# Kernel tuning notes

Hardware: AMD Instinct MI355X
Metric: run time of the kernel (lower is better)

The kernel has to match this reference:

```python
import jax, jax.numpy as jnp
import numpy as np

B, C, H, W = 32, 1024, 32, 32  # N = H*W must equal C for the attn_c * attn_s broadcast
C8 = C // 8


def setup_inputs() -> dict:
    key = jax.random.key(0)
    ks = jax.random.split(key, 9)
    s = 1.0 / np.sqrt(C)
    return {
        "z": jax.random.normal(ks[0], (B, C, H, W), jnp.float32),
        "x": jax.random.normal(ks[1], (B, C, H, W), jnp.float32),
        "y": jax.random.normal(ks[2], (B, C, H, W), jnp.float32),
        "Wq": jax.random.normal(ks[3], (C8, C), jnp.float32) * s,
        "bq": jax.random.normal(ks[4], (C8,), jnp.float32) * 0.01,
        "Wk": jax.random.normal(ks[5], (C8, C), jnp.float32) * s,
        "bk": jax.random.normal(ks[6], (C8,), jnp.float32) * 0.01,
        "Wv": jax.random.normal(ks[7], (C, C), jnp.float32) * s,
        "bv": jax.random.normal(ks[8], (C,), jnp.float32) * 0.01,
    }


def reference(z, x, y, Wq, bq, Wk, bk, Wv, bv):
    b, c, h, w = x.shape
    n = h * w
    xf = x.reshape(b, c, n)
    yf = y.reshape(b, c, n)
    zf = z.reshape(b, c, n)

    # 1x1 convs == channel matmuls
    q = jnp.einsum('oc,bcn->bon', Wq, xf) + bq[None, :, None]   # (B, C/8, N)
    k = jnp.einsum('oc,bcn->bon', Wk, yf) + bk[None, :, None]   # (B, C/8, N)

    # channel-projected spatial attention: (B, N, N)
    energy_c = jnp.einsum('bcn,bcm->bnm', q, k)
    attention_c = jax.nn.softmax(energy_c, axis=-1)

    # raw channel attention: (B, C, C)
    energy_s = jnp.einsum('bcn,bdn->bcd', xf, yf)
    energy_s = jnp.max(energy_s, axis=-1, keepdims=True) - energy_s
    attention_s = jax.nn.softmax(energy_s, axis=-1)

    # multiplicative combine + third softmax (requires N == C)
    attention = jax.nn.softmax(attention_c * attention_s, axis=-1)

    v = jnp.einsum('oc,bcn->bon', Wv, zf) + bv[None, :, None]   # (B, C, N)
    # out[b,c,m] = sum_n v[b,c,n] * attention[b,m,n]  (value @ attention^T)
    out = jnp.einsum('bcn,bmn->bcm', v, attention)
    return z + out.reshape(b, c, h, w)
```

## Files before the change

### kernel.cpp

```cpp
#include <hip/hip_runtime.h>
#include <hip/hip_bf16.h>

typedef __attribute__((ext_vector_type(8))) short s8_t;
typedef __attribute__((ext_vector_type(4))) float f4_t;

__device__ __forceinline__ unsigned short f2bf(float f) {
  union { float f; unsigned u; } x; x.f = f;
  unsigned r = x.u + 0x7fffu + ((x.u >> 16) & 1u);
  return (unsigned short)(r >> 16);
}

__device__ __forceinline__ void split1(float v, unsigned short& h, unsigned short& l) {
  unsigned b = __float_as_uint(v);
  unsigned hb = b & 0xFFFF0000u;
  h = (unsigned short)(b >> 16);
  float lo = v - __uint_as_float(hb);
  l = (unsigned short)(__float_as_uint(lo) >> 16);
}

__device__ __forceinline__ void split2(float e0, float e1, unsigned& hp, unsigned& lp) {
  unsigned b0 = __float_as_uint(e0), b1 = __float_as_uint(e1);
  unsigned h0 = b0 & 0xFFFF0000u, h1 = b1 & 0xFFFF0000u;
  hp = (b0 >> 16) | h1;
  float l0 = e0 - __uint_as_float(h0), l1 = e1 - __uint_as_float(h1);
  lp = (__float_as_uint(l0) >> 16) | (__float_as_uint(l1) & 0xFFFF0000u);
}

__device__ __forceinline__ void gload16(const void* g, void* l) {
  __builtin_amdgcn_global_load_lds(
      (const __attribute__((address_space(1))) void*)g,
      (__attribute__((address_space(3))) void*)l, 16, 0, 0);
}

__device__ __forceinline__ void swz_grid(int& bx, int& by, int& bz) {
  const int gx = gridDim.x, gy = gridDim.y;
  const int nwg = gx * gy * gridDim.z;
  const int flat = (blockIdx.z * gy + blockIdx.y) * gx + blockIdx.x;
  const int s = (flat & 7) * (nwg >> 3) + (flat >> 3);
  bx = s % gx;
  const int r = s / gx;
  by = r % gy;
  bz = r / gy;
}

__global__ __launch_bounds__(256) void k_convert(const float* __restrict__ in,
                                                 unsigned short* __restrict__ out, int n) {
  int i = (blockIdx.x * 256 + threadIdx.x) * 8;
  if (i >= n) return;
  float4 a = *(const float4*)(in + i);
  float4 b = *(const float4*)(in + i + 4);
  ushort4 u0; u0.x = f2bf(a.x); u0.y = f2bf(a.y); u0.z = f2bf(a.z); u0.w = f2bf(a.w);
  ushort4 u1; u1.x = f2bf(b.x); u1.y = f2bf(b.y); u1.z = f2bf(b.z); u1.w = f2bf(b.w);
  *(ushort4*)(out + i) = u0;
  *(ushort4*)(out + i + 4) = u1;
}

__global__ __launch_bounds__(256) void k_tsplitT(const float* __restrict__ in,
                                                 unsigned short* __restrict__ th,
                                                 unsigned short* __restrict__ tl) {
  __shared__ float tile[64][65];
  const int t = threadIdx.x, bz = blockIdx.z;
  const int r0 = blockIdx.y * 64, c0 = blockIdx.x * 64;
  const float* ip = in + (size_t)bz * 1048576;
  const size_t ob = (size_t)bz * 1048576;
  const int tr = t >> 4, tc = (t & 15) * 4;
#pragma unroll
  for (int p = 0; p < 4; ++p) {
    int r = p * 16 + tr;
    float4 v = *(const float4*)(ip + (size_t)(r0 + r) * 1024 + c0 + tc);
    tile[r][tc] = v.x; tile[r][tc + 1] = v.y; tile[r][tc + 2] = v.z; tile[r][tc + 3] = v.w;
  }
  __syncthreads();
#pragma unroll
  for (int p = 0; p < 4; ++p) {
    int n = p * 16 + tr;
    float a = tile[tc][n], b = tile[tc + 1][n], c = tile[tc + 2][n], d = tile[tc + 3][n];
    ushort4 h, l;
    split1(a, h.x, l.x); split1(b, h.y, l.y); split1(c, h.z, l.z); split1(d, h.w, l.w);
    *(ushort4*)(th + ob + (size_t)(c0 + n) * 1024 + r0 + tc) = h;
    *(ushort4*)(tl + ob + (size_t)(c0 + n) * 1024 + r0 + tc) = l;
  }
}

__global__ __launch_bounds__(256) void k_transpbf(const float* __restrict__ in,
                                                  unsigned short* __restrict__ outt) {
  __shared__ unsigned short tile[64][72];
  const int t = threadIdx.x, b = blockIdx.z;
  const int r0 = blockIdx.y * 64, c0 = blockIdx.x * 64;
  const float* ip = in + (size_t)b * 1048576;
  const int tr = t >> 4, tc = (t & 15) * 4;
#pragma unroll
  for (int p = 0; p < 4; ++p) {
    int r = p * 16 + tr;
    float4 v = *(const float4*)(ip + (size_t)(r0 + r) * 1024 + c0 + tc);
    tile[r][tc] = f2bf(v.x); tile[r][tc + 1] = f2bf(v.y);
    tile[r][tc + 2] = f2bf(v.z); tile[r][tc + 3] = f2bf(v.w);
  }
  __syncthreads();
#pragma unroll
  for (int p = 0; p < 4; ++p) {
    int n = p * 16 + tr;
    ushort4 w;
    w.x = tile[tc][n]; w.y = tile[tc + 1][n]; w.z = tile[tc + 2][n]; w.w = tile[tc + 3][n];
    *(ushort4*)(outt + (size_t)b * 1048576 + (size_t)(c0 + n) * 1024 + r0 + tc) = w;
  }
}

__device__ __forceinline__ void split_write(unsigned short* buf, int wbase,
                                            const float* av, const float* bv) {
  unsigned ah[8], al[8], bh[8], bl[8];
#pragma unroll
  for (int p = 0; p < 8; ++p) {
    split2(av[2 * p], av[2 * p + 1], ah[p], al[p]);
    split2(bv[2 * p], bv[2 * p + 1], bh[p], bl[p]);
  }
  *(uint4*)(buf + wbase) = *(uint4*)(ah);
  *(uint4*)(buf + wbase + 8) = *(uint4*)(ah + 4);
  *(uint4*)(buf + 4096 + wbase) = *(uint4*)(al);
  *(uint4*)(buf + 4096 + wbase + 8) = *(uint4*)(al + 4);
  *(uint4*)(buf + 8192 + wbase) = *(uint4*)(bh);
  *(uint4*)(buf + 8192 + wbase + 8) = *(uint4*)(bh + 4);
  *(uint4*)(buf + 12288 + wbase) = *(uint4*)(bl);
  *(uint4*)(buf + 12288 + wbase + 8) = *(uint4*)(bl + 4);
}

template <int BIAS_MODE>
__global__ __launch_bounds__(256) void k_mfma3(
    const float* __restrict__ A, int lda, long long sA,
    const float* __restrict__ B, int ldb, long long sB,
    float* __restrict__ C, int ldc, long long sC,
    const float* __restrict__ bias, int K) {
  __shared__ __align__(16) unsigned short sm[16384];
  int bxs, bys, bz; swz_grid(bxs, bys, bz);
  const int tid = threadIdx.x;
  const int lane = tid & 63, wave = tid >> 6;
  const int wr = wave >> 1, wc = wave & 1;
  const int m0 = bxs * 128, n0 = bys * 128;

  const int sr = tid >> 1, sh = (tid & 1) * 16;
  const float* ag = A + (long long)bz * sA + (long long)(m0 + sr) * lda + sh;
  const float* bg = B + (long long)bz * sB + (long long)(n0 + sr) * ldb + sh;
  const int wbase = sr * 32 + sh;

  const int lr = lane & 15, lg = lane >> 4;
  const int fa = (wr * 64 + lr) * 32 + lg * 8;
  const int fb = (wc * 64 + lr) * 32 + lg * 8;

  f4_t acc[4][4];
#pragma unroll
  for (int i = 0; i < 4; ++i)
#pragma unroll
    for (int j = 0; j < 4; ++j) acc[i][j] = (f4_t)0.f;

  for (int k0 = 0; k0 < K; k0 += 32) {
    float av[16], bv[16];
#pragma unroll
    for (int p = 0; p < 4; ++p) {
      *(float4*)(av + p * 4) = *(const float4*)(ag + p * 4);
      *(float4*)(bv + p * 4) = *(const float4*)(bg + p * 4);
    }
    split_write(sm, wbase, av, bv);
    ag += 32; bg += 32;
    __syncthreads();
    const unsigned short* Ahp = sm;
    const unsigned short* Alp = sm + 4096;
    const unsigned short* Bhp = sm + 8192;
    const unsigned short* Blp = sm + 12288;
    s8_t fah[4], fbh[4], ftmp[4];
#pragma unroll
    for (int f = 0; f < 4; ++f) {
      fah[f] = *(const s8_t*)(Ahp + fa + f * 512);
      fbh[f] = *(const s8_t*)(Bhp + fb + f * 512);
    }
#pragma unroll
    for (int i = 0; i < 4; ++i)
#pragma unroll
      for (int j = 0; j < 4; ++j)
        acc[i][j] = __builtin_amdgcn_mfma_f32_16x16x32_bf16(fah[i], fbh[j], acc[i][j], 0, 0, 0);
#pragma unroll
    for (int f = 0; f < 4; ++f) ftmp[f] = *(const s8_t*)(Blp + fb + f * 512);
#pragma unroll
    for (int i = 0; i < 4; ++i)
#pragma unroll
      for (int j = 0; j < 4; ++j)
        acc[i][j] = __builtin_amdgcn_mfma_f32_16x16x32_bf16(fah[i], ftmp[j], acc[i][j], 0, 0, 0);
#pragma unroll
    for (int f = 0; f < 4; ++f) ftmp[f] = *(const s8_t*)(Alp + fa + f * 512);
#pragma unroll
    for (int i = 0; i < 4; ++i)
#pragma unroll
      for (int j = 0; j < 4; ++j)
        acc[i][j] = __builtin_amdgcn_mfma_f32_16x16x32_bf16(ftmp[i], fbh[j], acc[i][j], 0, 0, 0);
    __syncthreads();
  }

#pragma unroll
  for (int i = 0; i < 4; ++i) {
    const int rbase = m0 + wr * 64 + i * 16 + lg * 4;
#pragma unroll
    for (int j = 0; j < 4; ++j) {
      const int col = n0 + wc * 64 + j * 16 + lr;
      float bc = (BIAS_MODE == 2) ? bias[col] : 0.f;
#pragma unroll
      for (int e = 0; e < 4; ++e) {
        float v = acc[i][j][e];
        if (BIAS_MODE == 2) v += bc;
        C[(long long)bz * sC + (long long)(rbase + e) * ldc + col] = v;
      }
    }
  }
}

__global__ __launch_bounds__(256) void k_qk3p(
    const unsigned short* __restrict__ Axh, const unsigned short* __restrict__ Axl,
    const unsigned short* __restrict__ Ayh, const unsigned short* __restrict__ Ayl,
    const float* __restrict__ Wqf, const float* __restrict__ Wkf,
    const float* __restrict__ bqf, const float* __restrict__ bkf,
    float* __restrict__ Qt, float* __restrict__ Kt) {
  __shared__ __align__(16) unsigned short smAh[4096], smAl[4096], smBh[4096], smBl[4096];
  int bx, by, bz; swz_grid(bx, by, bz);
  const unsigned short* Ah = by ? Ayh : Axh;
  const unsigned short* Al = by ? Ayl : Axl;
  const float* Bf = by ? Wkf : Wqf;
  const float* bias = by ? bkf : bqf;
  float* Of = by ? Kt : Qt;

  const int tid = threadIdx.x, lane = tid & 63, wave = tid >> 6;
  const int wr = wave >> 1, wc = wave & 1;
  const int m0 = bx * 128;

  const int ch0 = wave * 64 + lane, ch1 = ch0 + 256;
  const int r0 = ch0 >> 2, kc0 = (ch0 & 3) * 8, r1 = ch1 >> 2, kc1 = (ch1 & 3) * 8;
  const unsigned short* pah0 = Ah + (long long)bz * 1048576 + (long long)(m0 + r0) * 1024 + kc0;
  const unsigned short* pah1 = Ah + (long long)bz * 1048576 + (long long)(m0 + r1) * 1024 + kc1;
  const unsigned short* pal0 = Al + (long long)bz * 1048576 + (long long)(m0 + r0) * 1024 + kc0;
  const unsigned short* pal1 = Al + (long long)bz * 1048576 + (long long)(m0 + r1) * 1024 + kc1;
  char* dAh0 = (char*)smAh + wave * 1024; char* dAh1 = dAh0 + 4096;
  char* dAl0 = (char*)smAl + wave * 1024; char* dAl1 = dAl0 + 4096;

  const int sr = tid >> 1, sh = (tid & 1) * 16;
  const float* bg = Bf + (long long)sr * 1024 + sh;
  const int wbase = sr * 32 + sh;

  const int lr = lane & 15, lg = lane >> 4;
  const int fa = (wr * 64 + lr) * 32 + lg * 8;
  const int fb = (wc * 64 + lr) * 32 + lg * 8;

  f4_t acc[4][4];
#pragma unroll
  for (int i = 0; i < 4; ++i)
#pragma unroll
    for (int j = 0; j < 4; ++j) acc[i][j] = (f4_t)0.f;

  for (int k0 = 0; k0 < 1024; k0 += 32) {
    gload16(pah0, dAh0); gload16(pah1, dAh1);
    gload16(pal0, dAl0); gload16(pal1, dAl1);
    pah0 += 32; pah1 += 32; pal0 += 32; pal1 += 32;
    float bv[16];
#pragma unroll
    for (int p = 0; p < 4; ++p) *(float4*)(bv + p * 4) = *(const float4*)(bg + p * 4);
    bg += 32;
    unsigned bh[8], bl[8];
#pragma unroll
    for (int p = 0; p < 8; ++p) split2(bv[2 * p], bv[2 * p + 1], bh[p], bl[p]);
    *(uint4*)(smBh + wbase) = *(uint4*)(bh);
    *(uint4*)(smBh + wbase + 8) = *(uint4*)(bh + 4);
    *(uint4*)(smBl + wbase) = *(uint4*)(bl);
    *(uint4*)(smBl + wbase + 8) = *(uint4*)(bl + 4);
    __syncthreads();
    s8_t fah[4], fbh[4], ft[4];
#pragma unroll
    for (int f = 0; f < 4; ++f) {
      fah[f] = *(const s8_t*)(smAh + fa + f * 512);
      fbh[f] = *(const s8_t*)(smBh + fb + f * 512);
    }
#pragma unroll
    for (int i = 0; i < 4; ++i)
#pragma unroll
      for (int j = 0; j < 4; ++j)
        acc[i][j] = __builtin_amdgcn_mfma_f32_16x16x32_bf16(fah[i], fbh[j], acc[i][j], 0, 0, 0);
#pragma unroll
    for (int f = 0; f < 4; ++f) ft[f] = *(const s8_t*)(smBl + fb + f * 512);
#pragma unroll
    for (int i = 0; i < 4; ++i)
#pragma unroll
      for (int j = 0; j < 4; ++j)
        acc[i][j] = __builtin_amdgcn_mfma_f32_16x16x32_bf16(fah[i], ft[j], acc[i][j], 0, 0, 0);
#pragma unroll
    for (int f = 0; f < 4; ++f) ft[f] = *(const s8_t*)(smAl + fa + f * 512);
#pragma unroll
    for (int i = 0; i < 4; ++i)
#pragma unroll
      for (int j = 0; j < 4; ++j)
        acc[i][j] = __builtin_amdgcn_mfma_f32_16x16x32_bf16(ft[i], fbh[j], acc[i][j], 0, 0, 0);
    __syncthreads();
  }

#pragma unroll
  for (int i = 0; i < 4; ++i) {
    const int rbase = m0 + wr * 64 + i * 16 + lg * 4;
#pragma unroll
    for (int j = 0; j < 4; ++j) {
      const int col = wc * 64 + j * 16 + lr;
      const float bc = bias[col];
#pragma unroll
      for (int e = 0; e < 4; ++e)
        Of[(long long)bz * 131072 + (long long)(rbase + e) * 128 + col] = acc[i][j][e] + bc;
    }
  }
}

template <int BIAS_MODE, bool OUT_BF16, bool RESID>
__global__ __launch_bounds__(512) void k_mfma256(
    const unsigned short* __restrict__ A, int lda, long long sA,
    const unsigned short* __restrict__ B, int ldb, long long sB,
    void* __restrict__ Cp, int ldc, long long sC,
    const float* __restrict__ bias,
    const float* __restrict__ resid, long long sR, int K) {
  __shared__ __align__(16) unsigned short As[24576];
  __shared__ __align__(16) unsigned short Bs[24576];
  int bxs, bys, bz; swz_grid(bxs, bys, bz);
  const int tid = threadIdx.x;
  const int lane = tid & 63, wave = tid >> 6;
  const int wr = wave >> 2, wc = wave & 3;
  const int m0 = bxs * 256, n0 = bys * 256;

  const int cA0 = tid, cA1 = tid + 512;
  const unsigned short* pa0 = A + (long long)bz * sA + (long long)(m0 + (cA0 >> 2)) * lda + (cA0 & 3) * 8;
  const unsigned short* pa1 = A + (long long)bz * sA + (long long)(m0 + (cA1 >> 2)) * lda + (cA1 & 3) * 8;
  const unsigned short* pb0 = B + (long long)bz * sB + (long long)(n0 + (cA0 >> 2)) * ldb + (cA0 & 3) * 8;
  const unsigned short* pb1 = B + (long long)bz * sB + (long long)(n0 + (cA1 >> 2)) * ldb + (cA1 & 3) * 8;

  const int lr = lane & 15, lg = lane >> 4;
  const int fa = (wr * 128 + lr) * 32 + lg * 8;
  const int fb = (wc * 64 + lr) * 32 + lg * 8;

  f4_t acc[8][4];
#pragma unroll
  for (int i = 0; i < 8; ++i)
#pragma unroll
    for (int j = 0; j < 4; ++j) acc[i][j] = (f4_t)0.f;

  unsigned short* a0 = As; unsigned short* a1 = As + 8192; unsigned short* a2 = As + 16384;
  unsigned short* b0 = Bs; unsigned short* b1 = Bs + 8192; unsigned short* b2 = Bs + 16384;

  auto stage = [&](unsigned short* la, unsigned short* lb) {
    gload16(pa0, (char*)la + wave * 1024);
    gload16(pa1, (char*)la + 8192 + wave * 1024);
    gload16(pb0, (char*)lb + wave * 1024);
    gload16(pb1, (char*)lb + 8192 + wave * 1024);
    pa0 += 32; pa1 += 32; pb0 += 32; pb1 += 32;
  };

  const int nt = K >> 5;
  stage(a0, b0);
  stage(a1, b1);

  for (int t = 0; t < nt; ++t) {
    if (t + 2 < nt) {
      stage(a2, b2);
      asm volatile("s_waitcnt vmcnt(8)" ::: "memory");
    } else if (t + 1 < nt) {
      asm volatile("s_waitcnt vmcnt(4)" ::: "memory");
    } else {
      asm volatile("s_waitcnt vmcnt(0)" ::: "memory");
    }
    __builtin_amdgcn_sched_barrier(0);
    __builtin_amdgcn_s_barrier();
    __builtin_amdgcn_sched_barrier(0);
    const unsigned short* ap = a0;
    const unsigned short* bp = b0;
    s8_t af[8], bf[4];
#pragma unroll
    for (int i = 0; i < 8; ++i) af[i] = *(const s8_t*)(ap + fa + i * 512);
#pragma unroll
    for (int j = 0; j < 4; ++j) bf[j] = *(const s8_t*)(bp + fb + j * 512);
#pragma unroll
    for (int i = 0; i < 8; ++i)
#pragma unroll
      for (int j = 0; j < 4; ++j)
        acc[i][j] = __builtin_amdgcn_mfma_f32_16x16x32_bf16(af[i], bf[j], acc[i][j], 0, 0, 0);
    __builtin_amdgcn_sched_barrier(0);
    __builtin_amdgcn_s_barrier();
    __builtin_amdgcn_sched_barrier(0);
    unsigned short* ta = a0; a0 = a1; a1 = a2; a2 = ta;
    unsigned short* tb = b0; b0 = b1; b1 = b2; b2 = tb;
  }

#pragma unroll
  for (int i = 0; i < 8; ++i) {
    const int rbase = m0 + wr * 128 + i * 16 + lg * 4;
#pragma unroll
    for (int j = 0; j < 4; ++j) {
      const int col = n0 + wc * 64 + j * 16 + lr;
#pragma unroll
      for (int e = 0; e < 4; ++e) {
        const int row = rbase + e;
        float v = acc[i][j][e];
        if (BIAS_MODE == 1) v += bias[row];
        const long long off = (long long)bz * sC + (long long)row * ldc + col;
        if (RESID) v += resid[(long long)bz * sR + (long long)row * ldc + col];
        if (OUT_BF16) ((unsigned short*)Cp)[off] = f2bf(v);
        else          ((float*)Cp)[off] = v;
      }
    }
  }
}

__device__ __forceinline__ float wave_red_max(float v) {
#pragma unroll
  for (int o = 32; o > 0; o >>= 1) v = fmaxf(v, __shfl_down(v, o, 64));
  return v;
}
__device__ __forceinline__ float wave_red_sum(float v) {
#pragma unroll
  for (int o = 32; o > 0; o >>= 1) v += __shfl_down(v, o, 64);
  return v;
}
__device__ __forceinline__ float block_red_max(float v, float* red) {
  v = wave_red_max(v);
  if ((threadIdx.x & 63) == 0) red[threadIdx.x >> 6] = v;
  __syncthreads();
  v = fmaxf(fmaxf(red[0], red[1]), fmaxf(red[2], red[3]));
  __syncthreads();
  return v;
}
__device__ __forceinline__ float block_red_sum(float v, float* red) {
  v = wave_red_sum(v);
  if ((threadIdx.x & 63) == 0) red[threadIdx.x >> 6] = v;
  __syncthreads();
  v = red[0] + red[1] + red[2] + red[3];
  __syncthreads();
  return v;
}

__global__ __launch_bounds__(256) void k_combine(float* __restrict__ ec,
                                                 const float* __restrict__ es) {
  __shared__ float red[4];
  const size_t row = blockIdx.x;
  float* cp = ec + row * 1024;
  const float* sp = es + row * 1024;
  const int tid = threadIdx.x;
  float4 c4 = ((const float4*)cp)[tid];
  float4 s4 = ((const float4*)sp)[tid];

  float mx = fmaxf(fmaxf(c4.x, c4.y), fmaxf(c4.z, c4.w));
  mx = block_red_max(mx, red);
  float e0 = __expf(c4.x - mx), e1 = __expf(c4.y - mx);
  float e2 = __expf(c4.z - mx), e3 = __expf(c4.w - mx);
  float sc = block_red_sum(e0 + e1 + e2 + e3, red);

  float t0 = -s4.x, t1 = -s4.y, t2 = -s4.z, t3 = -s4.w;
  float mt = fmaxf(fmaxf(t0, t1), fmaxf(t2, t3));
  mt = block_red_max(mt, red);
  float f0 = __expf(t0 - mt), f1 = __expf(t1 - mt);
  float f2 = __expf(t2 - mt), f3 = __expf(t3 - mt);
  float ss = block_red_sum(f0 + f1 + f2 + f3, red);

  const float rc = 1.f / sc, rs = 1.f / ss;
  float g0 = __expf((e0 * rc) * (f0 * rs));
  float g1 = __expf((e1 * rc) * (f1 * rs));
  float g2 = __expf((e2 * rc) * (f2 * rs));
  float g3 = __expf((e3 * rc) * (f3 * rs));
  float s3 = block_red_sum(g0 + g1 + g2 + g3, red);
  const float r3 = 1.f / s3;
  ushort4 o;
  o.x = f2bf(g0 * r3); o.y = f2bf(g1 * r3); o.z = f2bf(g2 * r3); o.w = f2bf(g3 * r3);
  ((ushort4*)cp)[tid] = o;
}

extern "C" void kernel_launch(void* const* d_in, const int* in_sizes, int n_in,
                              void* d_out, int out_size, void* d_ws, size_t ws_size,
                              hipStream_t stream) {
  const float* z = (const float*)d_in[0];
  const float* x = (const float*)d_in[1];
  const float* y = (const float*)d_in[2];
  const float* Wq = (const float*)d_in[3];
  const float* bq = (const float*)d_in[4];
  const float* Wk = (const float*)d_in[5];
  const float* bk = (const float*)d_in[6];
  const float* Wv = (const float*)d_in[7];
  const float* bv = (const float*)d_in[8];
  float* out = (float*)d_out;

  char* ws = (char*)d_ws;
  unsigned short* yth = (unsigned short*)ws;
  unsigned short* ytl = yth + 33554432;
  float* es = (float*)ws;
  unsigned short* z_t = (unsigned short*)ws;
  unsigned short* v_bf = z_t + 33554432;
  char* wsB = ws + 134217728;
  unsigned short* xth = (unsigned short*)wsB;
  unsigned short* xtl = xth + 33554432;
  float* ec = (float*)wsB;
  unsigned short* attn = (unsigned short*)wsB;
  char* wsC = ws + 268435456;
  float* q_t = (float*)wsC;
  float* k_t = q_t + 4194304;
  unsigned short* wv = (unsigned short*)wsC;

  dim3 blk(256);
  hipLaunchKernelGGL(k_tsplitT, dim3(16, 16, 32), blk, 0, stream, x, xth, xtl);
  hipLaunchKernelGGL(k_tsplitT, dim3(16, 16, 32), blk, 0, stream, y, yth, ytl);
  hipLaunchKernelGGL(k_qk3p, dim3(8, 2, 32), blk, 0, stream,
                     xth, xtl, yth, ytl, Wq, Wk, bq, bk, q_t, k_t);
  hipLaunchKernelGGL((k_mfma3<0>), dim3(8, 8, 32), blk, 0, stream,
                     x, 1024, 1048576LL, y, 1024, 1048576LL, es, 1024, 1048576LL,
                     (const float*)nullptr, 1024);
  hipLaunchKernelGGL((k_mfma3<0>), dim3(8, 8, 32), blk, 0, stream,
                     q_t, 128, 131072LL, k_t, 128, 131072LL, ec, 1024, 1048576LL,
                     (const float*)nullptr, 128);
  hipLaunchKernelGGL(k_combine, dim3(32768), blk, 0, stream, ec, es);
  hipLaunchKernelGGL(k_transpbf, dim3(16, 16, 32), blk, 0, stream, z, z_t);
  hipLaunchKernelGGL(k_convert, dim3(512), blk, 0, stream, Wv, wv, 1048576);
  hipLaunchKernelGGL((k_mfma256<1, true, false>), dim3(4, 4, 32), dim3(512), 0, stream,
                     wv, 1024, 0LL, z_t, 1024, 1048576LL, (void*)v_bf, 1024, 1048576LL,
                     bv, (const float*)nullptr, 0LL, 1024);
  hipLaunchKernelGGL((k_mfma256<0, false, true>), dim3(4, 4, 32), dim3(512), 0, stream,
                     v_bf, 1024, 1048576LL, attn, 2048, 2097152LL, (void*)out, 1024, 1048576LL,
                     (const float*)nullptr, z, 1048576LL, 1024);
}
```

Before: 796.6 us.

## Double-buffer QK projection, deepen GEMM pipeline, use per-wave rows in combine

The QK projection kernel now double-buffers its A tiles in shared memory and prefetches the next weight slice while computing the current one, replacing the load-then-sync-then-compute loop. The 256-tile GEMM goes from a three-stage to a four-stage global-to-shared pipeline, raising shared-memory use to 128 KB per block. The combine softmax kernel now assigns one row per wave with xor-shuffle reductions, which removes the block-level shared-memory reductions and their barriers. The deeper buffering costs more LDS per block and may reduce occupancy.

```diff
diff --git a/kernel.cpp b/kernel.cpp
--- a/kernel.cpp
+++ b/kernel.cpp
@@ -217,7 +217,8 @@
     const float* __restrict__ Wqf, const float* __restrict__ Wkf,
     const float* __restrict__ bqf, const float* __restrict__ bkf,
     float* __restrict__ Qt, float* __restrict__ Kt) {
-  __shared__ __align__(16) unsigned short smAh[4096], smAl[4096], smBh[4096], smBl[4096];
+  __shared__ __align__(16) unsigned short smAh[8192], smAl[8192];
+  __shared__ __align__(16) unsigned short smBh[4096], smBl[4096];
   int bx, by, bz; swz_grid(bx, by, bz);
   const unsigned short* Ah = by ? Ayh : Axh;
   const unsigned short* Al = by ? Ayl : Axl;
@@ -235,8 +236,6 @@
   const unsigned short* pah1 = Ah + (long long)bz * 1048576 + (long long)(m0 + r1) * 1024 + kc1;
   const unsigned short* pal0 = Al + (long long)bz * 1048576 + (long long)(m0 + r0) * 1024 + kc0;
   const unsigned short* pal1 = Al + (long long)bz * 1048576 + (long long)(m0 + r1) * 1024 + kc1;
-  char* dAh0 = (char*)smAh + wave * 1024; char* dAh1 = dAh0 + 4096;
-  char* dAl0 = (char*)smAl + wave * 1024; char* dAl1 = dAl0 + 4096;
 
   const int sr = tid >> 1, sh = (tid & 1) * 16;
   const float* bg = Bf + (long long)sr * 1024 + sh;
@@ -252,14 +251,20 @@
 #pragma unroll
     for (int j = 0; j < 4; ++j) acc[i][j] = (f4_t)0.f;
 
-  for (int k0 = 0; k0 < 1024; k0 += 32) {
-    gload16(pah0, dAh0); gload16(pah1, dAh1);
-    gload16(pal0, dAl0); gload16(pal1, dAl1);
+  float bv[16];
+  auto stageA = [&](int b) {
+    char* dh = (char*)smAh + b * 8192 + wave * 1024;
+    char* dl = (char*)smAl + b * 8192 + wave * 1024;
+    gload16(pah0, dh); gload16(pah1, dh + 4096);
+    gload16(pal0, dl); gload16(pal1, dl + 4096);
     pah0 += 32; pah1 += 32; pal0 += 32; pal1 += 32;
-    float bv[16];
+  };
+  auto loadW = [&]() {
 #pragma unroll
     for (int p = 0; p < 4; ++p) *(float4*)(bv + p * 4) = *(const float4*)(bg + p * 4);
     bg += 32;
+  };
+  auto writeW = [&]() {
     unsigned bh[8], bl[8];
 #pragma unroll
     for (int p = 0; p < 8; ++p) split2(bv[2 * p], bv[2 * p + 1], bh[p], bl[p]);
@@ -267,11 +272,25 @@
     *(uint4*)(smBh + wbase + 8) = *(uint4*)(bh + 4);
     *(uint4*)(smBl + wbase) = *(uint4*)(bl);
     *(uint4*)(smBl + wbase + 8) = *(uint4*)(bl + 4);
-    __syncthreads();
+  };
+
+  stageA(0);
+  loadW();
+  writeW();
+  asm volatile("s_waitcnt vmcnt(0)" ::: "memory");
+  __builtin_amdgcn_sched_barrier(0);
+  __builtin_amdgcn_s_barrier();
+  __builtin_amdgcn_sched_barrier(0);
+
+  for (int t = 0; t < 32; ++t) {
+    const bool more = (t < 31);
+    if (more) { stageA((t + 1) & 1); loadW(); }
+    const unsigned short* Ahp = smAh + (t & 1) * 4096;
+    const unsigned short* Alp = smAl + (t & 1) * 4096;
     s8_t fah[4], fbh[4], ft[4];
 #pragma unroll
     for (int f = 0; f < 4; ++f) {
-      fah[f] = *(const s8_t*)(smAh + fa + f * 512);
+      fah[f] = *(const s8_t*)(Ahp + fa + f * 512);
       fbh[f] = *(const s8_t*)(smBh + fb + f * 512);
     }
 #pragma unroll
@@ -287,13 +306,22 @@
       for (int j = 0; j < 4; ++j)
         acc[i][j] = __builtin_amdgcn_mfma_f32_16x16x32_bf16(fah[i], ft[j], acc[i][j], 0, 0, 0);
 #pragma unroll
-    for (int f = 0; f < 4; ++f) ft[f] = *(const s8_t*)(smAl + fa + f * 512);
+    for (int f = 0; f < 4; ++f) ft[f] = *(const s8_t*)(Alp + fa + f * 512);
 #pragma unroll
     for (int i = 0; i < 4; ++i)
 #pragma unroll
       for (int j = 0; j < 4; ++j)
         acc[i][j] = __builtin_amdgcn_mfma_f32_16x16x32_bf16(ft[i], fbh[j], acc[i][j], 0, 0, 0);
-    __syncthreads();
+    __builtin_amdgcn_sched_barrier(0);
+    __builtin_amdgcn_s_barrier();
+    __builtin_amdgcn_sched_barrier(0);
+    if (more) {
+      writeW();
+      asm volatile("s_waitcnt vmcnt(0)" ::: "memory");
+    }
+    __builtin_amdgcn_sched_barrier(0);
+    __builtin_amdgcn_s_barrier();
+    __builtin_amdgcn_sched_barrier(0);
   }
 
 #pragma unroll
@@ -317,8 +345,8 @@
     void* __restrict__ Cp, int ldc, long long sC,
     const float* __restrict__ bias,
     const float* __restrict__ resid, long long sR, int K) {
-  __shared__ __align__(16) unsigned short As[24576];
-  __shared__ __align__(16) unsigned short Bs[24576];
+  __shared__ __align__(16) unsigned short As[32768];
+  __shared__ __align__(16) unsigned short Bs[32768];
   int bxs, bys, bz; swz_grid(bxs, bys, bz);
   const int tid = threadIdx.x;
   const int lane = tid & 63, wave = tid >> 6;
@@ -341,8 +369,10 @@
 #pragma unroll
     for (int j = 0; j < 4; ++j) acc[i][j] = (f4_t)0.f;
 
-  unsigned short* a0 = As; unsigned short* a1 = As + 8192; unsigned short* a2 = As + 16384;
-  unsigned short* b0 = Bs; unsigned short* b1 = Bs + 8192; unsigned short* b2 = Bs + 16384;
+  unsigned short* a0 = As;        unsigned short* a1 = As + 8192;
+  unsigned short* a2 = As + 16384; unsigned short* a3 = As + 24576;
+  unsigned short* b0 = Bs;        unsigned short* b1 = Bs + 8192;
+  unsigned short* b2 = Bs + 16384; unsigned short* b3 = Bs + 24576;
 
   auto stage = [&](unsigned short* la, unsigned short* lb) {
     gload16(pa0, (char*)la + wave * 1024);
@@ -355,10 +385,13 @@
   const int nt = K >> 5;
   stage(a0, b0);
   stage(a1, b1);
+  stage(a2, b2);
 
   for (int t = 0; t < nt; ++t) {
-    if (t + 2 < nt) {
-      stage(a2, b2);
+    if (t + 3 < nt) {
+      stage(a3, b3);
+      asm volatile("s_waitcnt vmcnt(12)" ::: "memory");
+    } else if (t + 2 < nt) {
       asm volatile("s_waitcnt vmcnt(8)" ::: "memory");
     } else if (t + 1 < nt) {
       asm volatile("s_waitcnt vmcnt(4)" ::: "memory");
@@ -383,8 +416,8 @@
     __builtin_amdgcn_sched_barrier(0);
     __builtin_amdgcn_s_barrier();
     __builtin_amdgcn_sched_barrier(0);
-    unsigned short* ta = a0; a0 = a1; a1 = a2; a2 = ta;
-    unsigned short* tb = b0; b0 = b1; b1 = b2; b2 = tb;
+    unsigned short* ta = a0; a0 = a1; a1 = a2; a2 = a3; a3 = ta;
+    unsigned short* tb = b0; b0 = b1; b1 = b2; b2 = b3; b3 = tb;
   }
 
 #pragma unroll
@@ -407,66 +440,75 @@
   }
 }
 
-__device__ __forceinline__ float wave_red_max(float v) {
-#pragma unroll
-  for (int o = 32; o > 0; o >>= 1) v = fmaxf(v, __shfl_down(v, o, 64));
+__device__ __forceinline__ float wred_max(float v) {
+#pragma unroll
+  for (int o = 1; o < 64; o <<= 1) v = fmaxf(v, __shfl_xor(v, o, 64));
   return v;
 }
-__device__ __forceinline__ float wave_red_sum(float v) {
-#pragma unroll
-  for (int o = 32; o > 0; o >>= 1) v += __shfl_down(v, o, 64);
-  return v;
-}
-__device__ __forceinline__ float block_red_max(float v, float* red) {
-  v = wave_red_max(v);
-  if ((threadIdx.x & 63) == 0) red[threadIdx.x >> 6] = v;
-  __syncthreads();
-  v = fmaxf(fmaxf(red[0], red[1]), fmaxf(red[2], red[3]));
-  __syncthreads();
-  return v;
-}
-__device__ __forceinline__ float block_red_sum(float v, float* red) {
-  v = wave_red_sum(v);
-  if ((threadIdx.x & 63) == 0) red[threadIdx.x >> 6] = v;
-  __syncthreads();
-  v = red[0] + red[1] + red[2] + red[3];
-  __syncthreads();
+__device__ __forceinline__ float wred_sum(float v) {
+#pragma unroll
+  for (int o = 1; o < 64; o <<= 1) v += __shfl_xor(v, o, 64);
   return v;
 }
 
 __global__ __launch_bounds__(256) void k_combine(float* __restrict__ ec,
                                                  const float* __restrict__ es) {
-  __shared__ float red[4];
-  const size_t row = blockIdx.x;
+  const int lane = threadIdx.x & 63, wid = threadIdx.x >> 6;
+  const size_t row = (size_t)blockIdx.x * 4 + wid;
   float* cp = ec + row * 1024;
   const float* sp = es + row * 1024;
-  const int tid = threadIdx.x;
-  float4 c4 = ((const float4*)cp)[tid];
-  float4 s4 = ((const float4*)sp)[tid];
-
-  float mx = fmaxf(fmaxf(c4.x, c4.y), fmaxf(c4.z, c4.w));
-  mx = block_red_max(mx, red);
-  float e0 = __expf(c4.x - mx), e1 = __expf(c4.y - mx);
-  float e2 = __expf(c4.z - mx), e3 = __expf(c4.w - mx);
-  float sc = block_red_sum(e0 + e1 + e2 + e3, red);
-
-  float t0 = -s4.x, t1 = -s4.y, t2 = -s4.z, t3 = -s4.w;
-  float mt = fmaxf(fmaxf(t0, t1), fmaxf(t2, t3));
-  mt = block_red_max(mt, red);
-  float f0 = __expf(t0 - mt), f1 = __expf(t1 - mt);
-  float f2 = __expf(t2 - mt), f3 = __expf(t3 - mt);
-  float ss = block_red_sum(f0 + f1 + f2 + f3, red);
-
+  float4 c[4], s[4];
+#pragma unroll
+  for (int p = 0; p < 4; ++p) {
+    c[p] = ((const float4*)cp)[lane * 4 + p];
+    s[p] = ((const float4*)sp)[lane * 4 + p];
+  }
+  float mx = -3.4e38f;
+#pragma unroll
+  for (int p = 0; p < 4; ++p)
+    mx = fmaxf(mx, fmaxf(fmaxf(c[p].x, c[p].y), fmaxf(c[p].z, c[p].w)));
+  mx = wred_max(mx);
+  float e[16], lsum = 0.f;
+#pragma unroll
+  for (int p = 0; p < 4; ++p) {
+    e[4 * p]     = __expf(c[p].x - mx);
+    e[4 * p + 1] = __expf(c[p].y - mx);
+    e[4 * p + 2] = __expf(c[p].z - mx);
+    e[4 * p + 3] = __expf(c[p].w - mx);
+    lsum += e[4 * p] + e[4 * p + 1] + e[4 * p + 2] + e[4 * p + 3];
+  }
+  const float sc = wred_sum(lsum);
+  float mt = -3.4e38f;
+#pragma unroll
+  for (int p = 0; p < 4; ++p)
+    mt = fmaxf(mt, fmaxf(fmaxf(-s[p].x, -s[p].y), fmaxf(-s[p].z, -s[p].w)));
+  mt = wred_max(mt);
+  float f[16]; lsum = 0.f;
+#pragma unroll
+  for (int p = 0; p < 4; ++p) {
+    f[4 * p]     = __expf(-s[p].x - mt);
+    f[4 * p + 1] = __expf(-s[p].y - mt);
+    f[4 * p + 2] = __expf(-s[p].z - mt);
+    f[4 * p + 3] = __expf(-s[p].w - mt);
+    lsum += f[4 * p] + f[4 * p + 1] + f[4 * p + 2] + f[4 * p + 3];
+  }
+  const float ss = wred_sum(lsum);
   const float rc = 1.f / sc, rs = 1.f / ss;
-  float g0 = __expf((e0 * rc) * (f0 * rs));
-  float g1 = __expf((e1 * rc) * (f1 * rs));
-  float g2 = __expf((e2 * rc) * (f2 * rs));
-  float g3 = __expf((e3 * rc) * (f3 * rs));
-  float s3 = block_red_sum(g0 + g1 + g2 + g3, red);
+  float g[16]; lsum = 0.f;
+#pragma unroll
+  for (int q = 0; q < 16; ++q) {
+    g[q] = __expf((e[q] * rc) * (f[q] * rs));
+    lsum += g[q];
+  }
+  const float s3 = wred_sum(lsum);
   const float r3 = 1.f / s3;
-  ushort4 o;
-  o.x = f2bf(g0 * r3); o.y = f2bf(g1 * r3); o.z = f2bf(g2 * r3); o.w = f2bf(g3 * r3);
-  ((ushort4*)cp)[tid] = o;
+#pragma unroll
+  for (int p = 0; p < 4; ++p) {
+    ushort4 o;
+    o.x = f2bf(g[4 * p] * r3);     o.y = f2bf(g[4 * p + 1] * r3);
+    o.z = f2bf(g[4 * p + 2] * r3); o.w = f2bf(g[4 * p + 3] * r3);
+    ((ushort4*)cp)[lane * 4 + p] = o;
+  }
 }
 
 extern "C" void kernel_launch(void* const* d_in, const int* in_sizes, int n_in,
@@ -510,7 +552,7 @@
   hipLaunchKernelGGL((k_mfma3<0>), dim3(8, 8, 32), blk, 0, stream,
                      q_t, 128, 131072LL, k_t, 128, 131072LL, ec, 1024, 1048576LL,
                      (const float*)nullptr, 128);
-  hipLaunchKernelGGL(k_combine, dim3(32768), blk, 0, stream, ec, es);
+  hipLaunchKernelGGL(k_combine, dim3(8192), blk, 0, stream, ec, es);
   hipLaunchKernelGGL(k_transpbf, dim3(16, 16, 32), blk, 0, stream, z, z_t);
   hipLaunchKernelGGL(k_convert, dim3(512), blk, 0, stream, Wv, wv, 1048576);
   hipLaunchKernelGGL((k_mfma256<1, true, false>), dim3(4, 4, 32), dim3(512), 0, stream,
```

New measurement: 801.7 us. About the same (+0.6%).
